# Optimization experiments

Measured on AMD Instinct MI355X. Metric: run time of the kernel, lower is better.

## Reference

```python
import jax, jax.numpy as jnp
import numpy as np

N_NODES = 50000
N_EDGES = 800000
IN_FEATS = 128
HID = 64
HEADS = 3
NUM_CLASSES = 8
ATTN_SLOPE = 0.2   # DGL GATConv leaky_relu slope on attention logits
ACT_SLOPE = 0.01   # nn.LeakyReLU default


def setup_inputs() -> dict:
    key = jax.random.key(0)
    ks = jax.random.split(key, 40)
    inp = {}
    inp["x"] = jax.random.normal(ks[0], (N_NODES, IN_FEATS), dtype=jnp.float32)
    inp["src"] = jax.random.randint(ks[1], (N_EDGES,), 0, N_NODES)
    inp["dst"] = jax.random.randint(ks[2], (N_EDGES,), 0, N_NODES)
    dims_in = [IN_FEATS, HID, HID, HID, HID]
    i = 3
    for l, din in enumerate(dims_in, start=1):
        inp[f"W{l}"] = jax.random.normal(ks[i], (din, HEADS * HID), dtype=jnp.float32) / np.float32(np.sqrt(din)); i += 1
        inp[f"b{l}"] = jnp.zeros((HEADS * HID,), dtype=jnp.float32)
        inp[f"al{l}"] = jax.random.normal(ks[i], (HEADS, HID), dtype=jnp.float32) * 0.1; i += 1
        inp[f"ar{l}"] = jax.random.normal(ks[i], (HEADS, HID), dtype=jnp.float32) * 0.1; i += 1
    inp["Wo"] = jax.random.normal(ks[i], (HID, NUM_CLASSES), dtype=jnp.float32) / np.float32(np.sqrt(HID)); i += 1
    inp["bo"] = jnp.zeros((NUM_CLASSES,), dtype=jnp.float32)
    return inp


def _gatconv(h, W, b, al, ar, src, dst):
    # h: [N, din] -> feat: [N, H, F]
    feat = (h @ W).reshape(N_NODES, HEADS, HID)
    el = jnp.einsum('nhf,hf->nh', feat, al)   # [N, H]
    er = jnp.einsum('nhf,hf->nh', feat, ar)   # [N, H]
    e = jax.nn.leaky_relu(el[src] + er[dst], ATTN_SLOPE)        # [E, H]
    # numerically-stable edge softmax segmented by destination node
    m = jax.ops.segment_max(e, dst, num_segments=N_NODES)      # [N, H]
    ex = jnp.exp(e - m[dst])                                   # [E, H]
    denom = jax.ops.segment_sum(ex, dst, num_segments=N_NODES)  # [N, H]
    alpha = ex / denom[dst]                                    # [E, H]
    msg = alpha[:, :, None] * feat[src]                        # [E, H, F]
    out = jax.ops.segment_sum(msg, dst, num_segments=N_NODES)  # [N, H, F]
    return out + b.reshape(HEADS, HID)


def reference(x, src, dst,
              W1, b1, al1, ar1,
              W2, b2, al2, ar2,
              W3, b3, al3, ar3,
              W4, b4, al4, ar4,
              W5, b5, al5, ar5,
              Wo, bo):
    layers = [(W1, b1, al1, ar1), (W2, b2, al2, ar2), (W3, b3, al3, ar3),
              (W4, b4, al4, ar4), (W5, b5, al5, ar5)]
    h = x
    for (W, b, al, ar) in layers:
        h = jax.nn.leaky_relu(_gatconv(h, W, b, al, ar, src, dst), ACT_SLOPE)
        h = h.mean(axis=1)  # mean over heads -> [N, F]
    return h @ Wo + bo      # [N, num_classes]
```

## Files before the change

kernel.cpp:

```cpp
#include <hip/hip_runtime.h>
#include <hip/hip_fp16.h>
#include <cstdint>

#define N_NODES 50000
#define N_EDGES 800000
#define IN_FEATS 128
#define HID 64
#define HEADS 3
#define NUM_CLASSES 8
#define ATTN_SLOPE 0.2f
#define ACT_SLOPE 0.01f

typedef _Float16 half8 __attribute__((ext_vector_type(8)));
typedef float f32x4 __attribute__((ext_vector_type(4)));

__device__ __forceinline__ float lrelu(float x, float s) { return x > 0.f ? x : s * x; }

__global__ void k_deg(const int* __restrict__ dst, int* __restrict__ deg, int E) {
    int i = blockIdx.x * blockDim.x + threadIdx.x;
    if (i < E) atomicAdd(&deg[dst[i]], 1);
}

__global__ __launch_bounds__(256) void k_scan1(const int* __restrict__ deg, int* __restrict__ off,
                                               int* __restrict__ bsum, int n) {
    __shared__ int wtot[4];
    int tid = threadIdx.x;
    int lane = tid & 63, wid = tid >> 6;
    int base = blockIdx.x * 2048 + tid * 8;
    int v[8];
    if (base + 8 <= n) {
        int4 a = *(const int4*)&deg[base];
        int4 b = *(const int4*)&deg[base + 4];
        v[0] = a.x; v[1] = a.y; v[2] = a.z; v[3] = a.w;
        v[4] = b.x; v[5] = b.y; v[6] = b.z; v[7] = b.w;
    } else {
#pragma unroll
        for (int j = 0; j < 8; ++j) v[j] = (base + j < n) ? deg[base + j] : 0;
    }
    int s[8];
    s[0] = v[0];
#pragma unroll
    for (int j = 1; j < 8; ++j) s[j] = s[j - 1] + v[j];
    int t = s[7];
    int incl = t;
    for (int o = 1; o < 64; o <<= 1) {
        int u = __shfl_up(incl, o);
        if (lane >= o) incl += u;
    }
    int excl = incl - t;
    if (lane == 63) wtot[wid] = incl;
    __syncthreads();
    int wprefix = 0;
    for (int w = 0; w < wid; ++w) wprefix += wtot[w];
    int base_off = wprefix + excl;
#pragma unroll
    for (int j = 0; j < 8; ++j)
        if (base + j < n) off[base + j] = base_off + s[j] - v[j];
    if (tid == 0) bsum[blockIdx.x] = wtot[0] + wtot[1] + wtot[2] + wtot[3];
}

__global__ __launch_bounds__(64) void k_scan2(int* __restrict__ bsum, int nb) {
    int tid = threadIdx.x;
    int v = (tid < nb) ? bsum[tid] : 0;
    int incl = v;
    for (int o = 1; o < 64; o <<= 1) {
        int u = __shfl_up(incl, o);
        if (tid >= o) incl += u;
    }
    if (tid < nb) bsum[tid] = incl - v;
}

__global__ __launch_bounds__(256) void k_scan3(int* __restrict__ off, const int* __restrict__ bsum,
                                               int n, int E) {
    int i = blockIdx.x * blockDim.x + threadIdx.x;
    if (i < n) off[i] += bsum[i >> 11];
    if (i == 0) off[n] = E;
}

__global__ void k_fill(const int* __restrict__ src, const int* __restrict__ dst,
                       const int* __restrict__ off, int* __restrict__ cur,
                       int* __restrict__ ssrc, int E) {
    int i = blockIdx.x * blockDim.x + threadIdx.x;
    if (i < E) {
        int d = dst[i];
        int p = atomicAdd(&cur[d], 1);
        ssrc[off[d] + p] = src[i];
    }
}

__global__ __launch_bounds__(256) void k_xcast(const float* __restrict__ x, _Float16* __restrict__ xh, int n8) {
    int i = blockIdx.x * blockDim.x + threadIdx.x;
    if (i < n8) {
        float4 a = *(const float4*)&x[i * 8];
        float4 b = *(const float4*)&x[i * 8 + 4];
        _Float16 v[8] = {(_Float16)a.x, (_Float16)a.y, (_Float16)a.z, (_Float16)a.w,
                         (_Float16)b.x, (_Float16)b.y, (_Float16)b.z, (_Float16)b.w};
        *(uint4*)&xh[i * 8] = *(uint4*)v;
    }
}

__global__ __launch_bounds__(256) void k_wcast(const float* __restrict__ W1, const float* __restrict__ W2,
                                               const float* __restrict__ W3, const float* __restrict__ W4,
                                               const float* __restrict__ W5, _Float16* __restrict__ Wt) {
    int i = blockIdx.x * blockDim.x + threadIdx.x;
    if (i >= 24576 + 4 * 12288) return;
    const float* W; int din; int idx; _Float16* out;
    if (i < 24576) { W = W1; din = 128; idx = i; out = Wt; }
    else {
        int j = i - 24576; int l = j / 12288; idx = j % 12288;
        W = (l == 0) ? W2 : (l == 1) ? W3 : (l == 2) ? W4 : W5;
        din = 64;
        out = Wt + 24576 + l * 12288;
    }
    int col = idx / din, k = idx % din;
    out[idx] = (_Float16)W[k * 192 + col];
}

__global__ __launch_bounds__(384) void k_gemm(const _Float16* __restrict__ h, const _Float16* __restrict__ Wt,
                                              const float* __restrict__ al, const float* __restrict__ ar,
                                              _Float16* __restrict__ feat,
                                              float* __restrict__ el, float* __restrict__ er,
                                              int N, int din) {
    __shared__ __align__(16) _Float16 Hl[128 * 72];
    __shared__ __align__(16) _Float16 Wl[192 * 72];
    const int LD = 72;
    int tid = threadIdx.x;
    int row0 = blockIdx.x * 128;
    int wid = tid >> 6, lane = tid & 63;
    int head = wid >> 1, rh = wid & 1;
    int c0 = head * 64;
    int l15 = lane & 15;
    int koff = (lane >> 4) * 8;
    int wr0 = rh * 64;

    f32x4 acc[4][4] = {};

    for (int k0 = 0; k0 < din; k0 += 64) {
        if (k0 > 0) __syncthreads();
        for (int i = tid; i < 192 * 8; i += 384) {
            int col = i >> 3, c8 = i & 7;
            *(uint4*)&Wl[col * LD + c8 * 8] = *(const uint4*)&Wt[(size_t)col * din + k0 + c8 * 8];
        }
        for (int i = tid; i < 128 * 8; i += 384) {
            int r = i >> 3, c8 = i & 7;
            int row = row0 + r;
            uint4 v = make_uint4(0, 0, 0, 0);
            if (row < N) v = *(const uint4*)&h[(size_t)row * din + k0 + c8 * 8];
            *(uint4*)&Hl[r * LD + c8 * 8] = v;
        }
        __syncthreads();

#pragma unroll
        for (int kb = 0; kb < 2; ++kb) {
            int kbase = kb * 32 + koff;
            half8 b0 = *(half8*)&Wl[(c0 + l15) * LD + kbase];
            half8 b1 = *(half8*)&Wl[(c0 + 16 + l15) * LD + kbase];
            half8 b2 = *(half8*)&Wl[(c0 + 32 + l15) * LD + kbase];
            half8 b3 = *(half8*)&Wl[(c0 + 48 + l15) * LD + kbase];
#pragma unroll
            for (int rt = 0; rt < 4; ++rt) {
                half8 a = *(half8*)&Hl[(wr0 + rt * 16 + l15) * LD + kbase];
                acc[rt][0] = __builtin_amdgcn_mfma_f32_16x16x32_f16(a, b0, acc[rt][0], 0, 0, 0);
                acc[rt][1] = __builtin_amdgcn_mfma_f32_16x16x32_f16(a, b1, acc[rt][1], 0, 0, 0);
                acc[rt][2] = __builtin_amdgcn_mfma_f32_16x16x32_f16(a, b2, acc[rt][2], 0, 0, 0);
                acc[rt][3] = __builtin_amdgcn_mfma_f32_16x16x32_f16(a, b3, acc[rt][3], 0, 0, 0);
            }
        }
    }

    float alv[4], arv[4];
#pragma unroll
    for (int ct = 0; ct < 4; ++ct) {
        alv[ct] = al[c0 + ct * 16 + l15];
        arv[ct] = ar[c0 + ct * 16 + l15];
    }

#pragma unroll
    for (int rt = 0; rt < 4; ++rt) {
#pragma unroll
        for (int r = 0; r < 4; ++r) {
            int row = row0 + wr0 + rt * 16 + (lane >> 4) * 4 + r;
            bool ok = (row < N);
            float c0v = acc[rt][0][r], c1v = acc[rt][1][r], c2v = acc[rt][2][r], c3v = acc[rt][3][r];
            if (ok) {
                size_t base = (size_t)row * 192 + c0;
                feat[base + l15]      = (_Float16)c0v;
                feat[base + 16 + l15] = (_Float16)c1v;
                feat[base + 32 + l15] = (_Float16)c2v;
                feat[base + 48 + l15] = (_Float16)c3v;
            }
            float pl = c0v * alv[0] + c1v * alv[1] + c2v * alv[2] + c3v * alv[3];
            float pr = c0v * arv[0] + c1v * arv[1] + c2v * arv[2] + c3v * arv[3];
            for (int o = 1; o < 16; o <<= 1) {
                pl += __shfl_xor(pl, o);
                pr += __shfl_xor(pr, o);
            }
            if (ok && l15 == 0) {
                el[row * HEADS + head] = pl;
                er[row * HEADS + head] = pr;
            }
        }
    }
}

__global__ __launch_bounds__(64) void k_agg(const int* __restrict__ off, const int* __restrict__ ssrc,
                                            const float* __restrict__ el, const float* __restrict__ er,
                                            const __half* __restrict__ feat, const float* __restrict__ b,
                                            __half* __restrict__ hout, int N) {
    __shared__ float4 ebuf[64];
    int wid = blockIdx.x;
    int lane = threadIdx.x;
    if (wid >= N) return;
    int start = off[wid], end = off[wid + 1];
    int cnt = end - start;
    float er0 = er[wid * HEADS + 0];
    float er1 = er[wid * HEADS + 1];
    float er2 = er[wid * HEADS + 2];
    float acc0 = 0.f, acc1 = 0.f, acc2 = 0.f;
    float den0 = 0.f, den1 = 0.f, den2 = 0.f;

    if (cnt <= 64) {
        int s0 = 0;
        float ea = -3.4e38f, eb = -3.4e38f, ec = -3.4e38f;
        if (lane < cnt) {
            s0 = ssrc[start + lane];
            ea = lrelu(el[s0 * HEADS + 0] + er0, ATTN_SLOPE);
            eb = lrelu(el[s0 * HEADS + 1] + er1, ATTN_SLOPE);
            ec = lrelu(el[s0 * HEADS + 2] + er2, ATTN_SLOPE);
        }
        float ma = ea, mb = eb, mc = ec;
        for (int o = 32; o > 0; o >>= 1) {
            ma = fmaxf(ma, __shfl_xor(ma, o));
            mb = fmaxf(mb, __shfl_xor(mb, o));
            mc = fmaxf(mc, __shfl_xor(mc, o));
        }
        float xa = (lane < cnt) ? __expf(ea - ma) : 0.f;
        float xb = (lane < cnt) ? __expf(eb - mb) : 0.f;
        float xc = (lane < cnt) ? __expf(ec - mc) : 0.f;
        float da = xa, db = xb, dc = xc;
        for (int o = 32; o > 0; o >>= 1) {
            da += __shfl_xor(da, o);
            db += __shfl_xor(db, o);
            dc += __shfl_xor(dc, o);
        }
        den0 = da; den1 = db; den2 = dc;
        ebuf[lane] = make_float4(__int_as_float(s0), xa, xb, xc);
        int t = 0;
        for (; t + 4 <= cnt; t += 4) {
            float4 v0 = ebuf[t + 0];
            float4 v1 = ebuf[t + 1];
            float4 v2 = ebuf[t + 2];
            float4 v3 = ebuf[t + 3];
            const __half* f0 = feat + (size_t)__float_as_int(v0.x) * 192 + lane;
            const __half* f1 = feat + (size_t)__float_as_int(v1.x) * 192 + lane;
            const __half* f2 = feat + (size_t)__float_as_int(v2.x) * 192 + lane;
            const __half* f3 = feat + (size_t)__float_as_int(v3.x) * 192 + lane;
            float p00 = __half2float(f0[0]), p01 = __half2float(f0[64]), p02 = __half2float(f0[128]);
            float p10 = __half2float(f1[0]), p11 = __half2float(f1[64]), p12 = __half2float(f1[128]);
            float p20 = __half2float(f2[0]), p21 = __half2float(f2[64]), p22 = __half2float(f2[128]);
            float p30 = __half2float(f3[0]), p31 = __half2float(f3[64]), p32 = __half2float(f3[128]);
            acc0 += v0.y * p00; acc1 += v0.z * p01; acc2 += v0.w * p02;
            acc0 += v1.y * p10; acc1 += v1.z * p11; acc2 += v1.w * p12;
            acc0 += v2.y * p20; acc1 += v2.z * p21; acc2 += v2.w * p22;
            acc0 += v3.y * p30; acc1 += v3.z * p31; acc2 += v3.w * p32;
        }
        for (; t < cnt; ++t) {
            float4 v = ebuf[t];
            const __half* fr = feat + (size_t)__float_as_int(v.x) * 192 + lane;
            acc0 += v.y * __half2float(fr[0]);
            acc1 += v.z * __half2float(fr[64]);
            acc2 += v.w * __half2float(fr[128]);
        }
    } else {
        float ma = -3.4e38f, mb = -3.4e38f, mc = -3.4e38f;
        for (int j = start + lane; j < end; j += 64) {
            int s = ssrc[j];
            ma = fmaxf(ma, lrelu(el[s * HEADS + 0] + er0, ATTN_SLOPE));
            mb = fmaxf(mb, lrelu(el[s * HEADS + 1] + er1, ATTN_SLOPE));
            mc = fmaxf(mc, lrelu(el[s * HEADS + 2] + er2, ATTN_SLOPE));
        }
        for (int o = 32; o > 0; o >>= 1) {
            ma = fmaxf(ma, __shfl_xor(ma, o));
            mb = fmaxf(mb, __shfl_xor(mb, o));
            mc = fmaxf(mc, __shfl_xor(mc, o));
        }
        float da = 0.f, db = 0.f, dc = 0.f;
        for (int j0 = start; j0 < end; j0 += 64) {
            int jj = j0 + lane;
            int s0 = 0;
            float xa = 0.f, xb = 0.f, xc = 0.f;
            if (jj < end) {
                s0 = ssrc[jj];
                xa = __expf(lrelu(el[s0 * HEADS + 0] + er0, ATTN_SLOPE) - ma);
                xb = __expf(lrelu(el[s0 * HEADS + 1] + er1, ATTN_SLOPE) - mb);
                xc = __expf(lrelu(el[s0 * HEADS + 2] + er2, ATTN_SLOPE) - mc);
            }
            da += xa; db += xb; dc += xc;
            ebuf[lane] = make_float4(__int_as_float(s0), xa, xb, xc);
            int c = min(64, end - j0);
            int t = 0;
            for (; t + 4 <= c; t += 4) {
                float4 v0 = ebuf[t + 0];
                float4 v1 = ebuf[t + 1];
                float4 v2 = ebuf[t + 2];
                float4 v3 = ebuf[t + 3];
                const __half* f0 = feat + (size_t)__float_as_int(v0.x) * 192 + lane;
                const __half* f1 = feat + (size_t)__float_as_int(v1.x) * 192 + lane;
                const __half* f2 = feat + (size_t)__float_as_int(v2.x) * 192 + lane;
                const __half* f3 = feat + (size_t)__float_as_int(v3.x) * 192 + lane;
                float p00 = __half2float(f0[0]), p01 = __half2float(f0[64]), p02 = __half2float(f0[128]);
                float p10 = __half2float(f1[0]), p11 = __half2float(f1[64]), p12 = __half2float(f1[128]);
                float p20 = __half2float(f2[0]), p21 = __half2float(f2[64]), p22 = __half2float(f2[128]);
                float p30 = __half2float(f3[0]), p31 = __half2float(f3[64]), p32 = __half2float(f3[128]);
                acc0 += v0.y * p00; acc1 += v0.z * p01; acc2 += v0.w * p02;
                acc0 += v1.y * p10; acc1 += v1.z * p11; acc2 += v1.w * p12;
                acc0 += v2.y * p20; acc1 += v2.z * p21; acc2 += v2.w * p22;
                acc0 += v3.y * p30; acc1 += v3.z * p31; acc2 += v3.w * p32;
            }
            for (; t < c; ++t) {
                float4 v = ebuf[t];
                const __half* fr = feat + (size_t)__float_as_int(v.x) * 192 + lane;
                acc0 += v.y * __half2float(fr[0]);
                acc1 += v.z * __half2float(fr[64]);
                acc2 += v.w * __half2float(fr[128]);
            }
        }
        for (int o = 32; o > 0; o >>= 1) {
            da += __shfl_xor(da, o);
            db += __shfl_xor(db, o);
            dc += __shfl_xor(dc, o);
        }
        den0 = da; den1 = db; den2 = dc;
    }

    float v0 = (cnt > 0) ? acc0 / den0 : 0.f;
    float v1 = (cnt > 0) ? acc1 / den1 : 0.f;
    float v2 = (cnt > 0) ? acc2 / den2 : 0.f;
    float hsum = lrelu(v0 + b[lane], ACT_SLOPE)
               + lrelu(v1 + b[64 + lane], ACT_SLOPE)
               + lrelu(v2 + b[128 + lane], ACT_SLOPE);
    hout[wid * 64 + lane] = __float2half(hsum * (1.f / 3.f));
}

__global__ __launch_bounds__(256) void k_out(const __half* __restrict__ h, const float* __restrict__ Wo,
                                             const float* __restrict__ bo, float* __restrict__ out, int N) {
    __shared__ float Hl[32][65];
    __shared__ float Wl[64 * 8];
    int tid = threadIdx.x;
    int n0 = blockIdx.x * 32;
    for (int i = tid; i < 32 * 64; i += 256) {
        int r = i >> 6, k = i & 63;
        Hl[r][k] = (n0 + r < N) ? __half2float(h[(n0 + r) * 64 + k]) : 0.f;
    }
    for (int i = tid; i < 512; i += 256) Wl[i] = Wo[i];
    __syncthreads();
    int r = tid >> 3, c = tid & 7;
    float acc = 0.f;
    for (int k = 0; k < 64; ++k) acc += Hl[r][k] * Wl[k * 8 + c];
    int row = n0 + r;
    if (row < N) out[row * 8 + c] = acc + bo[c];
}

extern "C" void kernel_launch(void* const* d_in, const int* in_sizes, int n_in,
                              void* d_out, int out_size, void* d_ws, size_t ws_size,
                              hipStream_t stream) {
    const float* x  = (const float*)d_in[0];
    const int* src  = (const int*)d_in[1];
    const int* dst  = (const int*)d_in[2];
    const float *W[5], *b[5], *al[5], *ar[5];
    for (int l = 0; l < 5; ++l) {
        W[l]  = (const float*)d_in[3 + l * 4];
        b[l]  = (const float*)d_in[4 + l * 4];
        al[l] = (const float*)d_in[5 + l * 4];
        ar[l] = (const float*)d_in[6 + l * 4];
    }
    const float* Wo = (const float*)d_in[23];
    const float* bo = (const float*)d_in[24];
    float* out = (float*)d_out;

    char* ws = (char*)d_ws;
    auto alloc = [&](size_t bytes) {
        char* p = ws;
        ws += (bytes + 255) & ~size_t(255);
        return p;
    };
    _Float16* feat = (_Float16*)alloc(sizeof(_Float16) * (size_t)N_NODES * 192);
    float* el      = (float*)alloc(sizeof(float) * (size_t)N_NODES * HEADS);
    float* er      = (float*)alloc(sizeof(float) * (size_t)N_NODES * HEADS);
    _Float16* xh   = (_Float16*)alloc(sizeof(_Float16) * (size_t)N_NODES * IN_FEATS);
    _Float16* h0   = (_Float16*)alloc(sizeof(_Float16) * (size_t)N_NODES * 64);
    _Float16* h1   = (_Float16*)alloc(sizeof(_Float16) * (size_t)N_NODES * 64);
    _Float16* wt   = (_Float16*)alloc(sizeof(_Float16) * (24576 + 4 * 12288));
    int* deg    = (int*)alloc(sizeof(int) * N_NODES);
    int* off    = (int*)alloc(sizeof(int) * (N_NODES + 1));
    int* cur    = (int*)alloc(sizeof(int) * N_NODES);
    int* ssrc   = (int*)alloc(sizeof(int) * N_EDGES);
    int* bsum   = (int*)alloc(sizeof(int) * 64);

    const int NB = (N_NODES + 2047) / 2048;
    (void)hipMemsetAsync(deg, 0, sizeof(int) * N_NODES, stream);
    (void)hipMemsetAsync(cur, 0, sizeof(int) * N_NODES, stream);
    k_deg<<<(N_EDGES + 255) / 256, 256, 0, stream>>>(dst, deg, N_EDGES);
    k_scan1<<<NB, 256, 0, stream>>>(deg, off, bsum, N_NODES);
    k_scan2<<<1, 64, 0, stream>>>(bsum, NB);
    k_scan3<<<(N_NODES + 255) / 256, 256, 0, stream>>>(off, bsum, N_NODES, N_EDGES);
    k_fill<<<(N_EDGES + 255) / 256, 256, 0, stream>>>(src, dst, off, cur, ssrc, N_EDGES);
    k_xcast<<<(N_NODES * IN_FEATS / 8 + 255) / 256, 256, 0, stream>>>(x, xh, N_NODES * IN_FEATS / 8);
    k_wcast<<<(24576 + 4 * 12288 + 255) / 256, 256, 0, stream>>>(W[0], W[1], W[2], W[3], W[4], wt);

    const _Float16* hin = xh;
    _Float16* hbuf[2] = {h0, h1};
    const _Float16* wts[5] = {wt, wt + 24576, wt + 24576 + 12288, wt + 24576 + 2 * 12288, wt + 24576 + 3 * 12288};
    int din = IN_FEATS;
    for (int l = 0; l < 5; ++l) {
        k_gemm<<<(N_NODES + 127) / 128, 384, 0, stream>>>(hin, wts[l], al[l], ar[l], feat, el, er, N_NODES, din);
        _Float16* hn = hbuf[l & 1];
        k_agg<<<N_NODES, 64, 0, stream>>>(off, ssrc, el, er,
                                          (const __half*)feat, b[l],
                                          (__half*)hn, N_NODES);
        hin = hn;
        din = HID;
    }
    k_out<<<(N_NODES + 31) / 32, 256, 0, stream>>>((const __half*)hin, Wo, bo, out, N_NODES);
}
```

Measured before the change: 521.7 us.

## Partition degree count and CSR fill atomics by destination node range

The degree-count and CSR-fill kernels now launch 8 node groups times 128 edge chunks. Each block scans one chunk of edges and only performs atomics for destinations in its group's node range. The likely aim is to confine each block's atomics to a smaller slice of the deg/cur arrays, giving better cache locality and probably landing that slice on fewer memory channels (the code does not tie groups to specific XCDs). In exchange every edge's dst is read 8 times and the fill adds divergent branches, while these kernels are a small share of total runtime.

```diff
diff --git a/kernel.cpp b/kernel.cpp
--- a/kernel.cpp
+++ b/kernel.cpp
@@ -11,14 +11,25 @@
 #define ATTN_SLOPE 0.2f
 #define ACT_SLOPE 0.01f
 
+#define NGRP 8
+#define GRP_NODES 6250
+#define NCHUNK 128
+#define CHUNK 6250
+
 typedef _Float16 half8 __attribute__((ext_vector_type(8)));
 typedef float f32x4 __attribute__((ext_vector_type(4)));
 
 __device__ __forceinline__ float lrelu(float x, float s) { return x > 0.f ? x : s * x; }
 
-__global__ void k_deg(const int* __restrict__ dst, int* __restrict__ deg, int E) {
-    int i = blockIdx.x * blockDim.x + threadIdx.x;
-    if (i < E) atomicAdd(&deg[dst[i]], 1);
+__global__ __launch_bounds__(256) void k_deg(const int* __restrict__ dst, int* __restrict__ deg, int E) {
+    int grp = blockIdx.x & (NGRP - 1);
+    int chunk = blockIdx.x >> 3;
+    int lo = grp * GRP_NODES, hi = lo + GRP_NODES;
+    int s = chunk * CHUNK, e = min(E, s + CHUNK);
+    for (int i = s + (int)threadIdx.x; i < e; i += 256) {
+        int d = dst[i];
+        if (d >= lo && d < hi) atomicAdd(&deg[d], 1);
+    }
 }
 
 __global__ __launch_bounds__(256) void k_scan1(const int* __restrict__ deg, int* __restrict__ off,
@@ -77,14 +88,19 @@
     if (i == 0) off[n] = E;
 }
 
-__global__ void k_fill(const int* __restrict__ src, const int* __restrict__ dst,
-                       const int* __restrict__ off, int* __restrict__ cur,
-                       int* __restrict__ ssrc, int E) {
-    int i = blockIdx.x * blockDim.x + threadIdx.x;
-    if (i < E) {
+__global__ __launch_bounds__(256) void k_fill(const int* __restrict__ src, const int* __restrict__ dst,
+                                              const int* __restrict__ off, int* __restrict__ cur,
+                                              int* __restrict__ ssrc, int E) {
+    int grp = blockIdx.x & (NGRP - 1);
+    int chunk = blockIdx.x >> 3;
+    int lo = grp * GRP_NODES, hi = lo + GRP_NODES;
+    int s = chunk * CHUNK, e = min(E, s + CHUNK);
+    for (int i = s + (int)threadIdx.x; i < e; i += 256) {
         int d = dst[i];
-        int p = atomicAdd(&cur[d], 1);
-        ssrc[off[d] + p] = src[i];
+        if (d >= lo && d < hi) {
+            int p = atomicAdd(&cur[d], 1);
+            ssrc[off[d] + p] = src[i];
+        }
     }
 }
 
@@ -400,11 +416,11 @@
     const int NB = (N_NODES + 2047) / 2048;
     (void)hipMemsetAsync(deg, 0, sizeof(int) * N_NODES, stream);
     (void)hipMemsetAsync(cur, 0, sizeof(int) * N_NODES, stream);
-    k_deg<<<(N_EDGES + 255) / 256, 256, 0, stream>>>(dst, deg, N_EDGES);
+    k_deg<<<NCHUNK * NGRP, 256, 0, stream>>>(dst, deg, N_EDGES);
     k_scan1<<<NB, 256, 0, stream>>>(deg, off, bsum, N_NODES);
     k_scan2<<<1, 64, 0, stream>>>(bsum, NB);
     k_scan3<<<(N_NODES + 255) / 256, 256, 0, stream>>>(off, bsum, N_NODES, N_EDGES);
-    k_fill<<<(N_EDGES + 255) / 256, 256, 0, stream>>>(src, dst, off, cur, ssrc, N_EDGES);
+    k_fill<<<NCHUNK * NGRP, 256, 0, stream>>>(src, dst, off, cur, ssrc, N_EDGES);
     k_xcast<<<(N_NODES * IN_FEATS / 8 + 255) / 256, 256, 0, stream>>>(x, xh, N_NODES * IN_FEATS / 8);
     k_wcast<<<(24576 + 4 * 12288 + 255) / 256, 256, 0, stream>>>(W[0], W[1], W[2], W[3], W[4], wt);
 
```

Result: no change. 516.8 us (-0.9%).
